# Kernel tuning notes

Hardware: AMD Instinct MI355X
Metric: run time of the kernel (lower is better)

The kernel has to match this reference:

```python
import jax, jax.numpy as jnp
import numpy as np

N, E, D, H_ATT = 10000, 640000, 128, 64


def setup_inputs() -> dict:
    key = jax.random.key(0)
    ks = jax.random.split(key, 8)
    s = 1.0 / np.sqrt(D)
    return {
        "x": jax.random.normal(ks[0], (N, D), jnp.float32),
        "row": jax.random.randint(ks[1], (E,), 0, N, dtype=jnp.int32),
        "col": jax.random.randint(ks[2], (E,), 0, N, dtype=jnp.int32),
        "W1": jax.random.normal(ks[3], (D, D), jnp.float32) * s,
        "b1": jnp.zeros((D,), jnp.float32),
        "W2": jax.random.normal(ks[4], (D, D), jnp.float32) * s,
        "b2": jnp.zeros((D,), jnp.float32),
        "A1": jax.random.normal(ks[5], (D, H_ATT), jnp.float32) * s,
        "ab1": jnp.zeros((H_ATT,), jnp.float32),
        "A2": jax.random.normal(ks[6], (H_ATT, 1), jnp.float32) * (1.0 / np.sqrt(H_ATT)),
    }


def _cos_sim(a, b):
    # torch.cosine_similarity with eps=1e-8
    num = jnp.sum(a * b, axis=-1)
    den = jnp.maximum(jnp.linalg.norm(a, axis=-1) * jnp.linalg.norm(b, axis=-1), 1e-8)
    return num / den


def _euclid(a, b):
    # nn.PairwiseDistance(p=2)
    return jnp.sqrt(jnp.sum((a - b) ** 2, axis=-1) + 1e-12)


def _gcn(x, ew, row, col, W, b):
    # PyG GCNConv: add self loops (weight 1), symmetric normalization, SpMM.
    n = x.shape[0]
    loop = jnp.arange(n, dtype=row.dtype)
    r = jnp.concatenate([row, loop])  # target
    c = jnp.concatenate([col, loop])  # source
    w = jnp.concatenate([ew, jnp.ones((n,), x.dtype)])
    deg = jax.ops.segment_sum(w, r, num_segments=n)
    dis = jnp.where(deg > 0, jax.lax.rsqrt(jnp.maximum(deg, 1e-12)), 0.0)
    norm = dis[r] * w * dis[c]  # [E+N]
    h = x @ W  # [N, out]
    out = jax.ops.segment_sum(norm[:, None] * h[c], r, num_segments=n)
    return out + b


def reference(x, row, col, W1, b1, W2, b2, A1, ab1, A2):
    # --- cosine branch ---
    w = _cos_sim(x[row], x[col])
    x1 = jax.nn.relu(_gcn(x, w, row, col, W1, b1))
    w = _cos_sim(x1[row], x1[col])
    x1 = _gcn(x1, w, row, col, W2, b2)
    # --- euclidean branch ---
    w = _euclid(x[row], x[col])
    x2 = jax.nn.relu(_gcn(x, w, row, col, W1, b1))
    w = _euclid(x2[row], x2[col])
    x2 = _gcn(x2, w, row, col, W2, b2)
    # --- semantic attention fusion ---
    emb = jnp.stack([x1, x2], axis=1)  # [N, 2, D]
    score = jnp.tanh(emb @ A1 + ab1) @ A2  # [N, 2, 1]
    beta = jax.nn.softmax(score, axis=1)
    return jnp.sum(beta * emb, axis=1)  # [N, D]
```

## Files before the change

### kernel.cpp

```cpp
#include <hip/hip_runtime.h>
#include <cstdint>
#include <cstddef>

#define DF 128
#define HATT 64
#define SL 64
#define RPB 1280

static inline int divup(int a, int b) { return (a + b - 1) / b; }

typedef int vint4 __attribute__((ext_vector_type(4)));
typedef unsigned short vus4 __attribute__((ext_vector_type(4)));

static __device__ __forceinline__ unsigned short f2bf(float f) {
    unsigned int u = __float_as_uint(f);
    u = (u + 0x7FFFu + ((u >> 16) & 1u)) >> 16;
    return (unsigned short)u;
}
static __device__ __forceinline__ float bf2f(unsigned short b) {
    return __uint_as_float(((unsigned int)b) << 16);
}

__global__ __launch_bounds__(256) void hist2_kernel(const int* __restrict__ row,
                                                    int* __restrict__ cnt2,
                                                    int E, int n, int ranges, int rpb, int es) {
    int rb = blockIdx.x % ranges;
    int s  = blockIdx.x / ranges;
    int lo = rb * rpb, hi = min(lo + rpb, n);
    int rows = hi - lo;
    __shared__ int lc[RPB];
    for (int j = threadIdx.x; j < rows; j += 256) lc[j] = 0;
    __syncthreads();
    int i0 = s * es, i1 = min(i0 + es, E);
    const vint4* rv = (const vint4*)row;
    for (int j = i0 / 4 + threadIdx.x; j < i1 / 4; j += 256) {
        vint4 r4 = __builtin_nontemporal_load(rv + j);
        if (r4.x >= lo && r4.x < hi) atomicAdd(&lc[r4.x - lo], 1);
        if (r4.y >= lo && r4.y < hi) atomicAdd(&lc[r4.y - lo], 1);
        if (r4.z >= lo && r4.z < hi) atomicAdd(&lc[r4.z - lo], 1);
        if (r4.w >= lo && r4.w < hi) atomicAdd(&lc[r4.w - lo], 1);
    }
    __syncthreads();
    for (int j = threadIdx.x; j < rows; j += 256) cnt2[(size_t)s * n + lo + j] = lc[j];
}

__global__ __launch_bounds__(256) void scanRT_kernel(int* __restrict__ cnt2,
                                                     int* __restrict__ tot, int n) {
    __shared__ int tile[SL][65];
    int r0 = blockIdx.x * 64;
    int w = threadIdx.x >> 6;
    int lane = threadIdx.x & 63;
    int rows = min(64, n - r0);
    for (int s = w; s < SL; s += 4) {
        int v = (lane < rows) ? cnt2[(size_t)s * n + r0 + lane] : 0;
        tile[s][lane] = v;
    }
    __syncthreads();
    int t = threadIdx.x;
    if (t < rows) {
        int run = 0;
#pragma unroll
        for (int s = 0; s < SL; ++s) {
            int v = tile[s][t];
            tile[s][t] = run;
            run += v;
        }
        tot[r0 + t] = run;
    }
    __syncthreads();
    for (int s = w; s < SL; s += 4) {
        if (lane < rows) cnt2[(size_t)s * n + r0 + lane] = tile[s][lane];
    }
}

__global__ __launch_bounds__(1024) void scanT_kernel(const int* __restrict__ tot,
                                                     int* __restrict__ row_ptr, int n) {
    __shared__ int sums[1024];
    int t = threadIdx.x;
    int chunk = (n + 1023) >> 10;
    int start = t * chunk, end = min(start + chunk, n);
    int s = 0;
    for (int r = start; r < end; ++r) s += tot[r];
    sums[t] = s;
    __syncthreads();
    for (int off = 1; off < 1024; off <<= 1) {
        int v = (t >= off) ? sums[t - off] : 0;
        __syncthreads();
        sums[t] += v;
        __syncthreads();
    }
    int run = sums[t] - s;
    for (int r = start; r < end; ++r) {
        row_ptr[r] = run;
        run += tot[r];
    }
    if (t == 1023) row_ptr[n] = sums[1023];
}

__global__ __launch_bounds__(256) void scatter2_kernel(const int* __restrict__ row,
                                                       const int* __restrict__ col,
                                                       const int* __restrict__ cnt2,
                                                       const int* __restrict__ row_ptr,
                                                       unsigned short* __restrict__ col_s,
                                                       int E, int n, int ranges, int rpb, int es) {
    int rb = blockIdx.x % ranges;
    int s  = blockIdx.x / ranges;
    int lo = rb * rpb, hi = min(lo + rpb, n);
    int rows = hi - lo;
    __shared__ int cur[RPB];
    for (int j = threadIdx.x; j < rows; j += 256)
        cur[j] = cnt2[(size_t)s * n + lo + j] + row_ptr[lo + j];
    __syncthreads();
    int i0 = s * es, i1 = min(i0 + es, E);
    const vint4* rv = (const vint4*)row;
    const vint4* cv = (const vint4*)col;
    for (int j = i0 / 4 + threadIdx.x; j < i1 / 4; j += 256) {
        vint4 r4 = __builtin_nontemporal_load(rv + j);
        bool b0 = (r4.x >= lo && r4.x < hi);
        bool b1 = (r4.y >= lo && r4.y < hi);
        bool b2 = (r4.z >= lo && r4.z < hi);
        bool b3 = (r4.w >= lo && r4.w < hi);
        if (b0 | b1 | b2 | b3) {
            vint4 c4 = __builtin_nontemporal_load(cv + j);
            if (b0) { int p = atomicAdd(&cur[r4.x - lo], 1); col_s[p] = (unsigned short)c4.x; }
            if (b1) { int p = atomicAdd(&cur[r4.y - lo], 1); col_s[p] = (unsigned short)c4.y; }
            if (b2) { int p = atomicAdd(&cur[r4.z - lo], 1); col_s[p] = (unsigned short)c4.z; }
            if (b3) { int p = atomicAdd(&cur[r4.w - lo], 1); col_s[p] = (unsigned short)c4.w; }
        }
    }
}

__global__ __launch_bounds__(256) void split_x_kernel(const float* __restrict__ x,
                                                      float* __restrict__ xA,
                                                      float* __restrict__ xB,
                                                      float* __restrict__ sqn, int n) {
    int wid = (blockIdx.x * blockDim.x + threadIdx.x) >> 6;
    int lane = threadIdx.x & 63;
    if (wid >= n) return;
    float v0 = x[(size_t)wid * DF + lane];
    float v1 = x[(size_t)wid * DF + 64 + lane];
    xA[(size_t)wid * 64 + lane] = v0;
    xB[(size_t)wid * 64 + lane] = v1;
    float s = v0 * v0 + v1 * v1;
    for (int off = 32; off; off >>= 1) s += __shfl_xor(s, off);
    if (lane == 0) sqn[wid] = s;
}

__global__ __launch_bounds__(256) void edgewA_kernel(const float* __restrict__ tA,
                                                     const unsigned short* __restrict__ col_s,
                                                     const int* __restrict__ row_ptr,
                                                     float* __restrict__ dpart, int n) {
    int wid = (blockIdx.x * blockDim.x + threadIdx.x) >> 6;
    int lane = threadIdx.x & 63;
    if (wid >= n) return;
    int sub = lane & 15, g = lane >> 4;
    int s = row_ptr[wid], e = row_ptr[wid + 1];
    float4 a = ((const float4*)(tA + (size_t)wid * 64))[sub];
    for (int base = s; base < e; base += 64) {
        int m = e - base; if (m > 64) m = 64;
        int cc = 0;
        if (lane < m) cc = (int)col_s[base + lane];
        float dkeep = 0.f;
#define EWA_BODY(CHK)                                                        \
        _Pragma("unroll")                                                    \
        for (int it = 0; it < 16; ++it) {                                    \
            int idx = g * 16 + it;                                           \
            int c = __shfl(cc, idx);                                         \
            if (CHK) {                                                       \
                float4 b = ((const float4*)(tA + (size_t)c * 64))[sub];      \
                float d = a.x * b.x + a.y * b.y + a.z * b.z + a.w * b.w;     \
                d += __shfl_xor(d, 8); d += __shfl_xor(d, 4);                \
                d += __shfl_xor(d, 2); d += __shfl_xor(d, 1);                \
                dkeep = (sub == it) ? d : dkeep;                             \
            }                                                                \
        }
        if (m == 64) { EWA_BODY(true) } else { EWA_BODY(idx < m) }
#undef EWA_BODY
        if (lane < m) dpart[base + lane] = dkeep;
    }
}

__global__ __launch_bounds__(256) void edgewB1_kernel(const float* __restrict__ tB,
                                                      const float* __restrict__ sqn,
                                                      const unsigned short* __restrict__ col_s,
                                                      const int* __restrict__ row_ptr,
                                                      const float* __restrict__ dpart,
                                                      float* __restrict__ wA,
                                                      float* __restrict__ wB,
                                                      float* __restrict__ disA,
                                                      float* __restrict__ disB, int n) {
    int wid = (blockIdx.x * blockDim.x + threadIdx.x) >> 6;
    int lane = threadIdx.x & 63;
    if (wid >= n) return;
    int sub = lane & 15, g = lane >> 4;
    int s = row_ptr[wid], e = row_ptr[wid + 1];
    float4 a = ((const float4*)(tB + (size_t)wid * 64))[sub];
    float na = sqn[wid];
    float accA = 0.f, accB = 0.f;
    for (int base = s; base < e; base += 64) {
        int m = e - base; if (m > 64) m = 64;
        int cc = 0; float dp = 0.f;
        if (lane < m) {
            cc = (int)col_s[base + lane];
            dp = dpart[base + lane];
        }
        float dkeep = 0.f;
#define EWB1_BODY(CHK)                                                       \
        _Pragma("unroll")                                                    \
        for (int it = 0; it < 16; ++it) {                                    \
            int idx = g * 16 + it;                                           \
            int c = __shfl(cc, idx);                                         \
            if (CHK) {                                                       \
                float4 b = ((const float4*)(tB + (size_t)c * 64))[sub];      \
                float d = a.x * b.x + a.y * b.y + a.z * b.z + a.w * b.w;     \
                d += __shfl_xor(d, 8); d += __shfl_xor(d, 4);                \
                d += __shfl_xor(d, 2); d += __shfl_xor(d, 1);                \
                dkeep = (sub == it) ? d : dkeep;                             \
            }                                                                \
        }
        if (m == 64) { EWB1_BODY(true) } else { EWB1_BODY(idx < m) }
#undef EWB1_BODY
        if (lane < m) {
            float d = dkeep + dp;
            float nb = sqn[cc];
            float cw = d / fmaxf(sqrtf(na * nb), 1e-8f);
            float ew = sqrtf(fmaxf(na + nb - 2.f * d, 0.f) + 1e-12f);
            wA[base + lane] = cw;
            wB[base + lane] = ew;
            accA += cw;
            accB += ew;
        }
    }
#pragma unroll
    for (int off = 32; off; off >>= 1) {
        accA += __shfl_xor(accA, off);
        accB += __shfl_xor(accB, off);
    }
    if (lane == 0) {
        float dA = 1.f + accA;
        disA[wid] = (dA > 0.f) ? rsqrtf(fmaxf(dA, 1e-12f)) : 0.f;
        float dB = 1.f + accB;
        disB[wid] = (dB > 0.f) ? rsqrtf(fmaxf(dB, 1e-12f)) : 0.f;
    }
}

__global__ __launch_bounds__(256) void edgewA2_kernel(const float* __restrict__ t0,
                                                      const float* __restrict__ t1,
                                                      const unsigned short* __restrict__ col_s,
                                                      const int* __restrict__ row_ptr,
                                                      float* __restrict__ dp0,
                                                      float* __restrict__ dp1, int n) {
    int br = blockIdx.x & 1;
    int wid = (blockIdx.x >> 1) * 4 + (threadIdx.x >> 6);
    int lane = threadIdx.x & 63;
    if (wid >= n) return;
    const float* tA = br ? t1 : t0;
    float* dpart = br ? dp1 : dp0;
    int sub = lane & 15, g = lane >> 4;
    int s = row_ptr[wid], e = row_ptr[wid + 1];
    float4 a = ((const float4*)(tA + (size_t)wid * 64))[sub];
    for (int base = s; base < e; base += 64) {
        int m = e - base; if (m > 64) m = 64;
        int cc = 0;
        if (lane < m) cc = (int)col_s[base + lane];
        float dkeep = 0.f;
#define EWA2_BODY(CHK)                                                       \
        _Pragma("unroll")                                                    \
        for (int it = 0; it < 16; ++it) {                                    \
            int idx = g * 16 + it;                                           \
            int c = __shfl(cc, idx);                                         \
            if (CHK) {                                                       \
                float4 b = ((const float4*)(tA + (size_t)c * 64))[sub];      \
                float d = a.x * b.x + a.y * b.y + a.z * b.z + a.w * b.w;     \
                d += __shfl_xor(d, 8); d += __shfl_xor(d, 4);                \
                d += __shfl_xor(d, 2); d += __shfl_xor(d, 1);                \
                dkeep = (sub == it) ? d : dkeep;                             \
            }                                                                \
        }
        if (m == 64) { EWA2_BODY(true) } else { EWA2_BODY(idx < m) }
#undef EWA2_BODY
        if (lane < m) dpart[base + lane] = dkeep;
    }
}

__global__ __launch_bounds__(256) void edgewB2_kernel(const float* __restrict__ t0B,
                                                      const float* __restrict__ t1B,
                                                      const float* __restrict__ sq1pA,
                                                      const float* __restrict__ sq1pB,
                                                      const float* __restrict__ sq2pA,
                                                      const float* __restrict__ sq2pB,
                                                      const unsigned short* __restrict__ col_s,
                                                      const int* __restrict__ row_ptr,
                                                      const float* __restrict__ dp0,
                                                      const float* __restrict__ dp1,
                                                      float* __restrict__ wsA,
                                                      float* __restrict__ wsB,
                                                      float* __restrict__ disA,
                                                      float* __restrict__ disB, int n) {
    int br = blockIdx.x & 1;
    int wid = (blockIdx.x >> 1) * 4 + (threadIdx.x >> 6);
    int lane = threadIdx.x & 63;
    if (wid >= n) return;
    const float* tB = br ? t1B : t0B;
    const float* sqA = br ? sq2pA : sq1pA;
    const float* sqB = br ? sq2pB : sq1pB;
    const float* dpart = br ? dp1 : dp0;
    float* wOut = br ? wsB : wsA;
    float* disOut = br ? disB : disA;
    int sub = lane & 15, g = lane >> 4;
    int s = row_ptr[wid], e = row_ptr[wid + 1];
    float4 a = ((const float4*)(tB + (size_t)wid * 64))[sub];
    float na = sqA[wid] + sqB[wid];
    float acc = 0.f;
    for (int base = s; base < e; base += 64) {
        int m = e - base; if (m > 64) m = 64;
        int cc = 0; float dp = 0.f;
        if (lane < m) {
            cc = (int)col_s[base + lane];
            dp = dpart[base + lane];
        }
        float dkeep = 0.f;
#define EWB2_BODY(CHK)                                                       \
        _Pragma("unroll")                                                    \
        for (int it = 0; it < 16; ++it) {                                    \
            int idx = g * 16 + it;                                           \
            int c = __shfl(cc, idx);                                         \
            if (CHK) {                                                       \
                float4 b = ((const float4*)(tB + (size_t)c * 64))[sub];      \
                float d = a.x * b.x + a.y * b.y + a.z * b.z + a.w * b.w;     \
                d += __shfl_xor(d, 8); d += __shfl_xor(d, 4);                \
                d += __shfl_xor(d, 2); d += __shfl_xor(d, 1);                \
                dkeep = (sub == it) ? d : dkeep;                             \
            }                                                                \
        }
        if (m == 64) { EWB2_BODY(true) } else { EWB2_BODY(idx < m) }
#undef EWB2_BODY
        if (lane < m) {
            float d = dkeep + dp;
            float nb = sqA[cc] + sqB[cc];
            float w;
            if (br == 0) w = d / fmaxf(sqrtf(na * nb), 1e-8f);
            else w = sqrtf(fmaxf(na + nb - 2.f * d, 0.f) + 1e-12f);
            wOut[base + lane] = w;
            acc += w;
        }
    }
#pragma unroll
    for (int off = 32; off; off >>= 1) acc += __shfl_xor(acc, off);
    if (lane == 0) {
        float dg = 1.f + acc;
        disOut[wid] = (dg > 0.f) ? rsqrtf(fmaxf(dg, 1e-12f)) : 0.f;
    }
}

__global__ __launch_bounds__(256) void mm_kernel(const float* __restrict__ inA,
                                                 const float* __restrict__ inB,
                                                 int strideIn,
                                                 const float* __restrict__ W,
                                                 unsigned short* __restrict__ hA,
                                                 unsigned short* __restrict__ hB, int n) {
    int wid = (blockIdx.x * blockDim.x + threadIdx.x) >> 6;
    int lane = threadIdx.x & 63;
    int i0 = wid * 4;
    if (i0 >= n) return;
    float v0[4], v1[4];
#pragma unroll
    for (int r = 0; r < 4; ++r) {
        int i = i0 + r;
        if (i < n) { v0[r] = inA[(size_t)i * strideIn + lane]; v1[r] = inB[(size_t)i * strideIn + lane]; }
        else { v0[r] = 0.f; v1[r] = 0.f; }
    }
    float acc0[4] = {0.f, 0.f, 0.f, 0.f};
    float acc1[4] = {0.f, 0.f, 0.f, 0.f};
#pragma unroll 4
    for (int k = 0; k < 64; ++k) {
        float w0 = W[k * DF + lane];
        float w1 = W[k * DF + 64 + lane];
#pragma unroll
        for (int r = 0; r < 4; ++r) {
            float a = __shfl(v0[r], k);
            acc0[r] = fmaf(a, w0, acc0[r]);
            acc1[r] = fmaf(a, w1, acc1[r]);
        }
    }
#pragma unroll 4
    for (int k = 0; k < 64; ++k) {
        float w0 = W[(k + 64) * DF + lane];
        float w1 = W[(k + 64) * DF + 64 + lane];
#pragma unroll
        for (int r = 0; r < 4; ++r) {
            float a = __shfl(v1[r], k);
            acc0[r] = fmaf(a, w0, acc0[r]);
            acc1[r] = fmaf(a, w1, acc1[r]);
        }
    }
#pragma unroll
    for (int r = 0; r < 4; ++r) {
        int i = i0 + r;
        if (i < n) {
            hA[(size_t)i * 64 + lane] = f2bf(acc0[r]);
            hB[(size_t)i * 64 + lane] = f2bf(acc1[r]);
        }
    }
}

__global__ __launch_bounds__(256) void mm2_kernel(const float* __restrict__ x1A_,
                                                  const float* __restrict__ x1B_,
                                                  const float* __restrict__ x2A_,
                                                  const float* __restrict__ x2B_,
                                                  const float* __restrict__ W,
                                                  unsigned short* __restrict__ h1A, unsigned short* __restrict__ h1B,
                                                  unsigned short* __restrict__ h2A, unsigned short* __restrict__ h2B,
                                                  int n) {
    int br = blockIdx.x & 1;
    const float* inA = br ? x2A_ : x1A_;
    const float* inB = br ? x2B_ : x1B_;
    unsigned short* hA = br ? h2A : h1A;
    unsigned short* hB = br ? h2B : h1B;
    int wid = (blockIdx.x >> 1) * 4 + (threadIdx.x >> 6);
    int lane = threadIdx.x & 63;
    int i0 = wid * 4;
    if (i0 >= n) return;
    float v0[4], v1[4];
#pragma unroll
    for (int r = 0; r < 4; ++r) {
        int i = i0 + r;
        if (i < n) { v0[r] = inA[(size_t)i * 64 + lane]; v1[r] = inB[(size_t)i * 64 + lane]; }
        else { v0[r] = 0.f; v1[r] = 0.f; }
    }
    float acc0[4] = {0.f, 0.f, 0.f, 0.f};
    float acc1[4] = {0.f, 0.f, 0.f, 0.f};
#pragma unroll 4
    for (int k = 0; k < 64; ++k) {
        float w0 = W[k * DF + lane];
        float w1 = W[k * DF + 64 + lane];
#pragma unroll
        for (int r = 0; r < 4; ++r) {
            float a = __shfl(v0[r], k);
            acc0[r] = fmaf(a, w0, acc0[r]);
            acc1[r] = fmaf(a, w1, acc1[r]);
        }
    }
#pragma unroll 4
    for (int k = 0; k < 64; ++k) {
        float w0 = W[(k + 64) * DF + lane];
        float w1 = W[(k + 64) * DF + 64 + lane];
#pragma unroll
        for (int r = 0; r < 4; ++r) {
            float a = __shfl(v1[r], k);
            acc0[r] = fmaf(a, w0, acc0[r]);
            acc1[r] = fmaf(a, w1, acc1[r]);
        }
    }
#pragma unroll
    for (int r = 0; r < 4; ++r) {
        int i = i0 + r;
        if (i < n) {
            hA[(size_t)i * 64 + lane] = f2bf(acc0[r]);
            hB[(size_t)i * 64 + lane] = f2bf(acc1[r]);
        }
    }
}

__global__ __launch_bounds__(256) void spmm_l1_kernel(const unsigned short* __restrict__ hA,
                                                      const unsigned short* __restrict__ hB,
                                                      const float* __restrict__ wsA,
                                                      const float* __restrict__ wsB,
                                                      const unsigned short* __restrict__ col_s,
                                                      const float* __restrict__ disA,
                                                      const float* __restrict__ disB,
                                                      const int* __restrict__ row_ptr,
                                                      const float* __restrict__ bias,
                                                      float* __restrict__ x1A, float* __restrict__ x1B,
                                                      float* __restrict__ x2A, float* __restrict__ x2B,
                                                      float* __restrict__ sq1pA, float* __restrict__ sq1pB,
                                                      float* __restrict__ sq2pA, float* __restrict__ sq2pB,
                                                      int n) {
    int half = blockIdx.x & 1;
    int wid = (blockIdx.x >> 1) * 4 + (threadIdx.x >> 6);
    int lane = threadIdx.x & 63;
    if (wid >= n) return;
    const unsigned short* hH = half ? hB : hA;
    float* x1H = half ? x1B : x1A;
    float* x2H = half ? x2B : x2A;
    float* sq1 = half ? sq1pB : sq1pA;
    float* sq2 = half ? sq2pB : sq2pA;
    const float* biasH = bias + half * 64;
    int sub = lane & 15, g = lane >> 4;
    int s = row_ptr[wid], e = row_ptr[wid + 1];
    float diA = disA[wid], diB = disB[wid];
    float4 aA = make_float4(0.f, 0.f, 0.f, 0.f);
    float4 aB = make_float4(0.f, 0.f, 0.f, 0.f);
    for (int base = s; base < e; base += 64) {
        int m = e - base; if (m > 64) m = 64;
        int cc = 0; float wa = 0.f, wb = 0.f;
        if (lane < m) {
            cc = (int)col_s[base + lane];
            wa = wsA[base + lane] * disA[cc];
            wb = wsB[base + lane] * disB[cc];
        }
#define SPL1_BODY(CHK)                                                       \
        _Pragma("unroll")                                                    \
        for (int it = 0; it < 16; ++it) {                                    \
            int idx = it * 4 + g;                                            \
            int c = __shfl(cc, idx);                                         \
            float ceA = __shfl(wa, idx);                                     \
            float ceB = __shfl(wb, idx);                                     \
            if (CHK) {                                                       \
                vus4 gv = ((const vus4*)(hH + (size_t)c * 64))[sub];         \
                float g0 = bf2f(gv.x), g1 = bf2f(gv.y);                      \
                float g2 = bf2f(gv.z), g3 = bf2f(gv.w);                      \
                aA.x = fmaf(ceA, g0, aA.x); aA.y = fmaf(ceA, g1, aA.y);      \
                aA.z = fmaf(ceA, g2, aA.z); aA.w = fmaf(ceA, g3, aA.w);      \
                aB.x = fmaf(ceB, g0, aB.x); aB.y = fmaf(ceB, g1, aB.y);      \
                aB.z = fmaf(ceB, g2, aB.z); aB.w = fmaf(ceB, g3, aB.w);      \
            }                                                                \
        }
        if (m == 64) { SPL1_BODY(true) } else { SPL1_BODY(idx < m) }
#undef SPL1_BODY
    }
#pragma unroll
    for (int off = 16; off <= 32; off <<= 1) {
        aA.x += __shfl_xor(aA.x, off); aA.y += __shfl_xor(aA.y, off);
        aA.z += __shfl_xor(aA.z, off); aA.w += __shfl_xor(aA.w, off);
        aB.x += __shfl_xor(aB.x, off); aB.y += __shfl_xor(aB.y, off);
        aB.z += __shfl_xor(aB.z, off); aB.w += __shfl_xor(aB.w, off);
    }
    vus4 hvb = ((const vus4*)(hH + (size_t)wid * 64))[sub];
    float4 hv = make_float4(bf2f(hvb.x), bf2f(hvb.y), bf2f(hvb.z), bf2f(hvb.w));
    float4 bb = ((const float4*)biasH)[sub];
    float4 oA, oB;
    oA.x = fmaxf(diA * (aA.x + diA * hv.x) + bb.x, 0.f);
    oA.y = fmaxf(diA * (aA.y + diA * hv.y) + bb.y, 0.f);
    oA.z = fmaxf(diA * (aA.z + diA * hv.z) + bb.z, 0.f);
    oA.w = fmaxf(diA * (aA.w + diA * hv.w) + bb.w, 0.f);
    oB.x = fmaxf(diB * (aB.x + diB * hv.x) + bb.x, 0.f);
    oB.y = fmaxf(diB * (aB.y + diB * hv.y) + bb.y, 0.f);
    oB.z = fmaxf(diB * (aB.z + diB * hv.z) + bb.z, 0.f);
    oB.w = fmaxf(diB * (aB.w + diB * hv.w) + bb.w, 0.f);
    if (g == 0) {
        ((float4*)(x1H + (size_t)wid * 64))[sub] = oA;
        ((float4*)(x2H + (size_t)wid * 64))[sub] = oB;
    }
    float sA = oA.x * oA.x + oA.y * oA.y + oA.z * oA.z + oA.w * oA.w;
    float sB = oB.x * oB.x + oB.y * oB.y + oB.z * oB.z + oB.w * oB.w;
#pragma unroll
    for (int off = 8; off; off >>= 1) {
        sA += __shfl_xor(sA, off);
        sB += __shfl_xor(sB, off);
    }
    if (lane == 0) { sq1[wid] = sA; sq2[wid] = sB; }
}

__global__ __launch_bounds__(256) void spmm2q_kernel(const unsigned short* __restrict__ h1A,
                                                     const unsigned short* __restrict__ h1B,
                                                     const unsigned short* __restrict__ h2A,
                                                     const unsigned short* __restrict__ h2B,
                                                     const float* __restrict__ wsA,
                                                     const float* __restrict__ wsB,
                                                     const unsigned short* __restrict__ col_s,
                                                     const float* __restrict__ disA,
                                                     const float* __restrict__ disB,
                                                     const int* __restrict__ row_ptr,
                                                     const float* __restrict__ bias,
                                                     float* __restrict__ x1A, float* __restrict__ x1B,
                                                     float* __restrict__ x2A, float* __restrict__ x2B,
                                                     int n) {
    int sel = blockIdx.x & 3;
    int br = sel & 1;
    int half = sel >> 1;
    const unsigned short* hH = br ? (half ? h2B : h2A) : (half ? h1B : h1A);
    const float* ws = br ? wsB : wsA;
    const float* dis = br ? disB : disA;
    float* outH = br ? (half ? x2B : x2A) : (half ? x1B : x1A);
    const float* biasH = bias + half * 64;
    int wid = (blockIdx.x >> 2) * 4 + (threadIdx.x >> 6);
    int lane = threadIdx.x & 63;
    if (wid >= n) return;
    int sub = lane & 15, g = lane >> 4;
    int s = row_ptr[wid], e = row_ptr[wid + 1];
    float di = dis[wid];
    float4 a = make_float4(0.f, 0.f, 0.f, 0.f);
    for (int base = s; base < e; base += 64) {
        int m = e - base; if (m > 64) m = 64;
        int cc = 0; float wv = 0.f;
        if (lane < m) {
            cc = (int)col_s[base + lane];
            wv = ws[base + lane] * dis[cc];
        }
#define SP2_BODY(CHK)                                                        \
        _Pragma("unroll")                                                    \
        for (int it = 0; it < 16; ++it) {                                    \
            int idx = it * 4 + g;                                            \
            int c = __shfl(cc, idx);                                         \
            float ce = __shfl(wv, idx);                                      \
            if (CHK) {                                                       \
                vus4 gv = ((const vus4*)(hH + (size_t)c * 64))[sub];         \
                a.x = fmaf(ce, bf2f(gv.x), a.x);                             \
                a.y = fmaf(ce, bf2f(gv.y), a.y);                             \
                a.z = fmaf(ce, bf2f(gv.z), a.z);                             \
                a.w = fmaf(ce, bf2f(gv.w), a.w);                             \
            }                                                                \
        }
        if (m == 64) { SP2_BODY(true) } else { SP2_BODY(idx < m) }
#undef SP2_BODY
    }
#pragma unroll
    for (int off = 16; off <= 32; off <<= 1) {
        a.x += __shfl_xor(a.x, off); a.y += __shfl_xor(a.y, off);
        a.z += __shfl_xor(a.z, off); a.w += __shfl_xor(a.w, off);
    }
    if (g == 0) {
        vus4 hvb = ((const vus4*)(hH + (size_t)wid * 64))[sub];
        float4 bb = ((const float4*)biasH)[sub];
        float4 o;
        o.x = di * (a.x + di * bf2f(hvb.x)) + bb.x;
        o.y = di * (a.y + di * bf2f(hvb.y)) + bb.y;
        o.z = di * (a.z + di * bf2f(hvb.z)) + bb.z;
        o.w = di * (a.w + di * bf2f(hvb.w)) + bb.w;
        ((float4*)(outH + (size_t)wid * 64))[sub] = o;
    }
}

__global__ __launch_bounds__(256) void attn_kernel(const float* __restrict__ x1A,
                                                   const float* __restrict__ x1B,
                                                   const float* __restrict__ x2A,
                                                   const float* __restrict__ x2B,
                                                   const float* __restrict__ A1,
                                                   const float* __restrict__ ab1,
                                                   const float* __restrict__ A2,
                                                   float* __restrict__ out, int n) {
    __shared__ float sA1[DF * HATT];
    __shared__ float sA2[HATT];
    __shared__ float sab[HATT];
    int tid = threadIdx.x;
    for (int i = tid; i < DF * HATT; i += 256) sA1[i] = A1[i];
    if (tid < HATT) { sA2[tid] = A2[tid]; sab[tid] = ab1[tid]; }
    __syncthreads();
    int lane = tid & 63;
    int wib = tid >> 6;
    int wid = blockIdx.x * 4 + wib;
    int nw = gridDim.x * 4;
    for (int i = wid; i < n; i += nw) {
        float u0 = x1A[(size_t)i * 64 + lane], u1 = x1B[(size_t)i * 64 + lane];
        float v0 = x2A[(size_t)i * 64 + lane], v1 = x2B[(size_t)i * 64 + lane];
        float acc1 = 0.f, acc2 = 0.f;
#pragma unroll 4
        for (int d = 0; d < 64; ++d) {
            float w = sA1[d * HATT + lane];
            acc1 = fmaf(__shfl(u0, d), w, acc1);
            acc2 = fmaf(__shfl(v0, d), w, acc2);
        }
#pragma unroll 4
        for (int d = 0; d < 64; ++d) {
            float w = sA1[(d + 64) * HATT + lane];
            acc1 = fmaf(__shfl(u1, d), w, acc1);
            acc2 = fmaf(__shfl(v1, d), w, acc2);
        }
        float t1 = tanhf(acc1 + sab[lane]) * sA2[lane];
        float t2 = tanhf(acc2 + sab[lane]) * sA2[lane];
        for (int off = 32; off; off >>= 1) {
            t1 += __shfl_xor(t1, off);
            t2 += __shfl_xor(t2, off);
        }
        float mx = fmaxf(t1, t2);
        float e1 = expf(t1 - mx), e2 = expf(t2 - mx);
        float inv = 1.f / (e1 + e2);
        float be1 = e1 * inv, be2 = e2 * inv;
        out[(size_t)i * DF + lane] = be1 * u0 + be2 * v0;
        out[(size_t)i * DF + 64 + lane] = be1 * u1 + be2 * v1;
    }
}


extern "C" void kernel_launch(void* const* d_in, const int* in_sizes, int n_in,
                              void* d_out, int out_size, void* d_ws, size_t ws_size,
                              hipStream_t stream) {
    const float* x  = (const float*)d_in[0];
    const int* row  = (const int*)d_in[1];
    const int* col  = (const int*)d_in[2];
    const float* W1 = (const float*)d_in[3];
    const float* b1 = (const float*)d_in[4];
    const float* W2 = (const float*)d_in[5];
    const float* b2 = (const float*)d_in[6];
    const float* A1 = (const float*)d_in[7];
    const float* ab1= (const float*)d_in[8];
    const float* A2 = (const float*)d_in[9];
    const int N = in_sizes[0] / DF;
    const int E = in_sizes[1];
    float* out = (float*)d_out;

    char* p = (char*)d_ws;
    auto alloc_b = [&](size_t bytes) -> char* {
        char* r = p;
        p += (bytes + 255) & ~(size_t)255;
        return r;
    };
    float* xA    = (float*)alloc_b((size_t)N * 64 * 4);
    float* xB    = (float*)alloc_b((size_t)N * 64 * 4);
    unsigned short* hA  = (unsigned short*)alloc_b((size_t)N * 64 * 2);
    unsigned short* hB  = (unsigned short*)alloc_b((size_t)N * 64 * 2);
    unsigned short* h2A = (unsigned short*)alloc_b((size_t)N * 64 * 2);
    unsigned short* h2B = (unsigned short*)alloc_b((size_t)N * 64 * 2);
    float* x1A   = (float*)alloc_b((size_t)N * 64 * 4);
    float* x1B   = (float*)alloc_b((size_t)N * 64 * 4);
    float* x2A   = (float*)alloc_b((size_t)N * 64 * 4);
    float* x2B   = (float*)alloc_b((size_t)N * 64 * 4);
    float* wsA   = (float*)alloc_b((size_t)E * 4);
    float* wsB   = (float*)alloc_b((size_t)E * 4);
    float* dp0   = (float*)alloc_b((size_t)E * 4);
    float* dp1   = (float*)alloc_b((size_t)E * 4);
    float* disA  = (float*)alloc_b((size_t)N * 4);
    float* disB  = (float*)alloc_b((size_t)N * 4);
    float* sqnx  = (float*)alloc_b((size_t)N * 4);
    float* sq1pA = (float*)alloc_b((size_t)N * 4);
    float* sq1pB = (float*)alloc_b((size_t)N * 4);
    float* sq2pA = (float*)alloc_b((size_t)N * 4);
    float* sq2pB = (float*)alloc_b((size_t)N * 4);
    int* cnt2    = (int*)alloc_b((size_t)SL * N * 4);
    int* tot     = (int*)alloc_b((size_t)N * 4);
    int* rowptr  = (int*)alloc_b((size_t)(N + 1) * 4);
    unsigned short* col_s = (unsigned short*)alloc_b((size_t)E * 2);
    (void)ws_size; (void)n_in; (void)out_size;

    const int nodeBlocks  = divup(N * 64, 256);
    const int pairBlocks  = 2 * nodeBlocks;
    const int quadBlocks  = 4 * nodeBlocks;
    const int mmBlocks    = divup(divup(N, 4), 4);
    const int mm2Blocks   = 2 * mmBlocks;
    const int ranges = divup(N, RPB);
    const int rpb    = divup(N, ranges);
    int es = divup(E, SL); es = (es + 3) & ~3;
    const int prepBlocks = ranges * SL;

    hist2_kernel<<<prepBlocks, 256, 0, stream>>>(row, cnt2, E, N, ranges, rpb, es);
    split_x_kernel<<<nodeBlocks, 256, 0, stream>>>(x, xA, xB, sqnx, N);
    scanRT_kernel<<<divup(N, 64), 256, 0, stream>>>(cnt2, tot, N);
    scanT_kernel<<<1, 1024, 0, stream>>>(tot, rowptr, N);
    scatter2_kernel<<<prepBlocks, 256, 0, stream>>>(row, col, cnt2, rowptr, col_s, E, N, ranges, rpb, es);

    mm_kernel<<<mmBlocks, 256, 0, stream>>>(x, x + 64, DF, W1, hA, hB, N);

    edgewA_kernel<<<nodeBlocks, 256, 0, stream>>>(xA, col_s, rowptr, dp0, N);
    edgewB1_kernel<<<nodeBlocks, 256, 0, stream>>>(xB, sqnx, col_s, rowptr, dp0,
                                                   wsA, wsB, disA, disB, N);

    spmm_l1_kernel<<<pairBlocks, 256, 0, stream>>>(hA, hB, wsA, wsB, col_s, disA, disB,
                                                   rowptr, b1, x1A, x1B, x2A, x2B,
                                                   sq1pA, sq1pB, sq2pA, sq2pB, N);

    edgewA2_kernel<<<pairBlocks, 256, 0, stream>>>(x1A, x2A, col_s, rowptr, dp0, dp1, N);
    edgewB2_kernel<<<pairBlocks, 256, 0, stream>>>(x1B, x2B, sq1pA, sq1pB, sq2pA, sq2pB,
                                                   col_s, rowptr, dp0, dp1,
                                                   wsA, wsB, disA, disB, N);

    mm2_kernel<<<mm2Blocks, 256, 0, stream>>>(x1A, x1B, x2A, x2B, W2, hA, hB, h2A, h2B, N);

    spmm2q_kernel<<<quadBlocks, 256, 0, stream>>>(hA, hB, h2A, h2B, wsA, wsB, col_s,
                                                  disA, disB, rowptr, b2,
                                                  x1A, x1B, x2A, x2B, N);

    attn_kernel<<<divup(N, 4), 256, 0, stream>>>(x1A, x1B, x2A, x2B, A1, ab1, A2, out, N);
}
```

Before: 356.8 us.

## Merge feature-half splits in SpMM kernels so each wave handles full rows

The layer-1 SpMM now has one wave per node gather both 64-wide halves of h and produce both branch outputs, instead of launching separate blocks per half. The layer-2 SpMM likewise goes from four blocks per node to two, each covering both halves. Squared norms are now reduced in-kernel into a single array per branch, so edgewB2 reads one value per node instead of summing two partials. This removes redundant loads of row_ptr, col indices and edge weights across the split launches, and the per-node partial-norm reads. In exchange it raises register pressure and per-wave work, and reduces the number of waves available to hide gather latency.

```diff
diff --git a/kernel.cpp b/kernel.cpp
--- a/kernel.cpp
+++ b/kernel.cpp
@@ -285,10 +285,8 @@
 
 __global__ __launch_bounds__(256) void edgewB2_kernel(const float* __restrict__ t0B,
                                                       const float* __restrict__ t1B,
-                                                      const float* __restrict__ sq1pA,
-                                                      const float* __restrict__ sq1pB,
-                                                      const float* __restrict__ sq2pA,
-                                                      const float* __restrict__ sq2pB,
+                                                      const float* __restrict__ sqn1,
+                                                      const float* __restrict__ sqn2,
                                                       const unsigned short* __restrict__ col_s,
                                                       const int* __restrict__ row_ptr,
                                                       const float* __restrict__ dp0,
@@ -302,15 +300,14 @@
     int lane = threadIdx.x & 63;
     if (wid >= n) return;
     const float* tB = br ? t1B : t0B;
-    const float* sqA = br ? sq2pA : sq1pA;
-    const float* sqB = br ? sq2pB : sq1pB;
+    const float* sq = br ? sqn2 : sqn1;
     const float* dpart = br ? dp1 : dp0;
     float* wOut = br ? wsB : wsA;
     float* disOut = br ? disB : disA;
     int sub = lane & 15, g = lane >> 4;
     int s = row_ptr[wid], e = row_ptr[wid + 1];
     float4 a = ((const float4*)(tB + (size_t)wid * 64))[sub];
-    float na = sqA[wid] + sqB[wid];
+    float na = sq[wid];
     float acc = 0.f;
     for (int base = s; base < e; base += 64) {
         int m = e - base; if (m > 64) m = 64;
@@ -337,7 +334,7 @@
 #undef EWB2_BODY
         if (lane < m) {
             float d = dkeep + dp;
-            float nb = sqA[cc] + sqB[cc];
+            float nb = sq[cc];
             float w;
             if (br == 0) w = d / fmaxf(sqrtf(na * nb), 1e-8f);
             else w = sqrtf(fmaxf(na + nb - 2.f * d, 0.f) + 1e-12f);
@@ -473,24 +470,18 @@
                                                       const float* __restrict__ bias,
                                                       float* __restrict__ x1A, float* __restrict__ x1B,
                                                       float* __restrict__ x2A, float* __restrict__ x2B,
-                                                      float* __restrict__ sq1pA, float* __restrict__ sq1pB,
-                                                      float* __restrict__ sq2pA, float* __restrict__ sq2pB,
+                                                      float* __restrict__ sqn1, float* __restrict__ sqn2,
                                                       int n) {
-    int half = blockIdx.x & 1;
-    int wid = (blockIdx.x >> 1) * 4 + (threadIdx.x >> 6);
+    int wid = (blockIdx.x * blockDim.x + threadIdx.x) >> 6;
     int lane = threadIdx.x & 63;
     if (wid >= n) return;
-    const unsigned short* hH = half ? hB : hA;
-    float* x1H = half ? x1B : x1A;
-    float* x2H = half ? x2B : x2A;
-    float* sq1 = half ? sq1pB : sq1pA;
-    float* sq2 = half ? sq2pB : sq2pA;
-    const float* biasH = bias + half * 64;
     int sub = lane & 15, g = lane >> 4;
     int s = row_ptr[wid], e = row_ptr[wid + 1];
     float diA = disA[wid], diB = disB[wid];
-    float4 aA = make_float4(0.f, 0.f, 0.f, 0.f);
-    float4 aB = make_float4(0.f, 0.f, 0.f, 0.f);
+    float4 a1A = make_float4(0.f, 0.f, 0.f, 0.f);
+    float4 a1B = make_float4(0.f, 0.f, 0.f, 0.f);
+    float4 a2A = make_float4(0.f, 0.f, 0.f, 0.f);
+    float4 a2B = make_float4(0.f, 0.f, 0.f, 0.f);
     for (int base = s; base < e; base += 64) {
         int m = e - base; if (m > 64) m = 64;
         int cc = 0; float wa = 0.f, wb = 0.f;
@@ -507,13 +498,20 @@
             float ceA = __shfl(wa, idx);                                     \
             float ceB = __shfl(wb, idx);                                     \
             if (CHK) {                                                       \
-                vus4 gv = ((const vus4*)(hH + (size_t)c * 64))[sub];         \
-                float g0 = bf2f(gv.x), g1 = bf2f(gv.y);                      \
-                float g2 = bf2f(gv.z), g3 = bf2f(gv.w);                      \
-                aA.x = fmaf(ceA, g0, aA.x); aA.y = fmaf(ceA, g1, aA.y);      \
-                aA.z = fmaf(ceA, g2, aA.z); aA.w = fmaf(ceA, g3, aA.w);      \
-                aB.x = fmaf(ceB, g0, aB.x); aB.y = fmaf(ceB, g1, aB.y);      \
-                aB.z = fmaf(ceB, g2, aB.z); aB.w = fmaf(ceB, g3, aB.w);      \
+                vus4 gA = ((const vus4*)(hA + (size_t)c * 64))[sub];         \
+                vus4 gB = ((const vus4*)(hB + (size_t)c * 64))[sub];         \
+                float fa0 = bf2f(gA.x), fa1 = bf2f(gA.y);                    \
+                float fa2 = bf2f(gA.z), fa3 = bf2f(gA.w);                    \
+                float fb0 = bf2f(gB.x), fb1 = bf2f(gB.y);                    \
+                float fb2 = bf2f(gB.z), fb3 = bf2f(gB.w);                    \
+                a1A.x = fmaf(ceA, fa0, a1A.x); a1A.y = fmaf(ceA, fa1, a1A.y);\
+                a1A.z = fmaf(ceA, fa2, a1A.z); a1A.w = fmaf(ceA, fa3, a1A.w);\
+                a1B.x = fmaf(ceA, fb0, a1B.x); a1B.y = fmaf(ceA, fb1, a1B.y);\
+                a1B.z = fmaf(ceA, fb2, a1B.z); a1B.w = fmaf(ceA, fb3, a1B.w);\
+                a2A.x = fmaf(ceB, fa0, a2A.x); a2A.y = fmaf(ceB, fa1, a2A.y);\
+                a2A.z = fmaf(ceB, fa2, a2A.z); a2A.w = fmaf(ceB, fa3, a2A.w);\
+                a2B.x = fmaf(ceB, fb0, a2B.x); a2B.y = fmaf(ceB, fb1, a2B.y);\
+                a2B.z = fmaf(ceB, fb2, a2B.z); a2B.w = fmaf(ceB, fb3, a2B.w);\
             }                                                                \
         }
         if (m == 64) { SPL1_BODY(true) } else { SPL1_BODY(idx < m) }
@@ -521,38 +519,57 @@
     }
 #pragma unroll
     for (int off = 16; off <= 32; off <<= 1) {
-        aA.x += __shfl_xor(aA.x, off); aA.y += __shfl_xor(aA.y, off);
-        aA.z += __shfl_xor(aA.z, off); aA.w += __shfl_xor(aA.w, off);
-        aB.x += __shfl_xor(aB.x, off); aB.y += __shfl_xor(aB.y, off);
-        aB.z += __shfl_xor(aB.z, off); aB.w += __shfl_xor(aB.w, off);
-    }
-    vus4 hvb = ((const vus4*)(hH + (size_t)wid * 64))[sub];
-    float4 hv = make_float4(bf2f(hvb.x), bf2f(hvb.y), bf2f(hvb.z), bf2f(hvb.w));
-    float4 bb = ((const float4*)biasH)[sub];
-    float4 oA, oB;
-    oA.x = fmaxf(diA * (aA.x + diA * hv.x) + bb.x, 0.f);
-    oA.y = fmaxf(diA * (aA.y + diA * hv.y) + bb.y, 0.f);
-    oA.z = fmaxf(diA * (aA.z + diA * hv.z) + bb.z, 0.f);
-    oA.w = fmaxf(diA * (aA.w + diA * hv.w) + bb.w, 0.f);
-    oB.x = fmaxf(diB * (aB.x + diB * hv.x) + bb.x, 0.f);
-    oB.y = fmaxf(diB * (aB.y + diB * hv.y) + bb.y, 0.f);
-    oB.z = fmaxf(diB * (aB.z + diB * hv.z) + bb.z, 0.f);
-    oB.w = fmaxf(diB * (aB.w + diB * hv.w) + bb.w, 0.f);
+        a1A.x += __shfl_xor(a1A.x, off); a1A.y += __shfl_xor(a1A.y, off);
+        a1A.z += __shfl_xor(a1A.z, off); a1A.w += __shfl_xor(a1A.w, off);
+        a1B.x += __shfl_xor(a1B.x, off); a1B.y += __shfl_xor(a1B.y, off);
+        a1B.z += __shfl_xor(a1B.z, off); a1B.w += __shfl_xor(a1B.w, off);
+        a2A.x += __shfl_xor(a2A.x, off); a2A.y += __shfl_xor(a2A.y, off);
+        a2A.z += __shfl_xor(a2A.z, off); a2A.w += __shfl_xor(a2A.w, off);
+        a2B.x += __shfl_xor(a2B.x, off); a2B.y += __shfl_xor(a2B.y, off);
+        a2B.z += __shfl_xor(a2B.z, off); a2B.w += __shfl_xor(a2B.w, off);
+    }
+    vus4 hvAb = ((const vus4*)(hA + (size_t)wid * 64))[sub];
+    vus4 hvBb = ((const vus4*)(hB + (size_t)wid * 64))[sub];
+    float4 hvA = make_float4(bf2f(hvAb.x), bf2f(hvAb.y), bf2f(hvAb.z), bf2f(hvAb.w));
+    float4 hvB = make_float4(bf2f(hvBb.x), bf2f(hvBb.y), bf2f(hvBb.z), bf2f(hvBb.w));
+    float4 bbA = ((const float4*)bias)[sub];
+    float4 bbB = ((const float4*)(bias + 64))[sub];
+    float4 o1A, o1B, o2A, o2B;
+    o1A.x = fmaxf(diA * (a1A.x + diA * hvA.x) + bbA.x, 0.f);
+    o1A.y = fmaxf(diA * (a1A.y + diA * hvA.y) + bbA.y, 0.f);
+    o1A.z = fmaxf(diA * (a1A.z + diA * hvA.z) + bbA.z, 0.f);
+    o1A.w = fmaxf(diA * (a1A.w + diA * hvA.w) + bbA.w, 0.f);
+    o1B.x = fmaxf(diA * (a1B.x + diA * hvB.x) + bbB.x, 0.f);
+    o1B.y = fmaxf(diA * (a1B.y + diA * hvB.y) + bbB.y, 0.f);
+    o1B.z = fmaxf(diA * (a1B.z + diA * hvB.z) + bbB.z, 0.f);
+    o1B.w = fmaxf(diA * (a1B.w + diA * hvB.w) + bbB.w, 0.f);
+    o2A.x = fmaxf(diB * (a2A.x + diB * hvA.x) + bbA.x, 0.f);
+    o2A.y = fmaxf(diB * (a2A.y + diB * hvA.y) + bbA.y, 0.f);
+    o2A.z = fmaxf(diB * (a2A.z + diB * hvA.z) + bbA.z, 0.f);
+    o2A.w = fmaxf(diB * (a2A.w + diB * hvA.w) + bbA.w, 0.f);
+    o2B.x = fmaxf(diB * (a2B.x + diB * hvB.x) + bbB.x, 0.f);
+    o2B.y = fmaxf(diB * (a2B.y + diB * hvB.y) + bbB.y, 0.f);
+    o2B.z = fmaxf(diB * (a2B.z + diB * hvB.z) + bbB.z, 0.f);
+    o2B.w = fmaxf(diB * (a2B.w + diB * hvB.w) + bbB.w, 0.f);
     if (g == 0) {
-        ((float4*)(x1H + (size_t)wid * 64))[sub] = oA;
-        ((float4*)(x2H + (size_t)wid * 64))[sub] = oB;
-    }
-    float sA = oA.x * oA.x + oA.y * oA.y + oA.z * oA.z + oA.w * oA.w;
-    float sB = oB.x * oB.x + oB.y * oB.y + oB.z * oB.z + oB.w * oB.w;
+        ((float4*)(x1A + (size_t)wid * 64))[sub] = o1A;
+        ((float4*)(x1B + (size_t)wid * 64))[sub] = o1B;
+        ((float4*)(x2A + (size_t)wid * 64))[sub] = o2A;
+        ((float4*)(x2B + (size_t)wid * 64))[sub] = o2B;
+    }
+    float s1 = o1A.x * o1A.x + o1A.y * o1A.y + o1A.z * o1A.z + o1A.w * o1A.w
+             + o1B.x * o1B.x + o1B.y * o1B.y + o1B.z * o1B.z + o1B.w * o1B.w;
+    float s2 = o2A.x * o2A.x + o2A.y * o2A.y + o2A.z * o2A.z + o2A.w * o2A.w
+             + o2B.x * o2B.x + o2B.y * o2B.y + o2B.z * o2B.z + o2B.w * o2B.w;
 #pragma unroll
     for (int off = 8; off; off >>= 1) {
-        sA += __shfl_xor(sA, off);
-        sB += __shfl_xor(sB, off);
-    }
-    if (lane == 0) { sq1[wid] = sA; sq2[wid] = sB; }
-}
-
-__global__ __launch_bounds__(256) void spmm2q_kernel(const unsigned short* __restrict__ h1A,
+        s1 += __shfl_xor(s1, off);
+        s2 += __shfl_xor(s2, off);
+    }
+    if (lane == 0) { sqn1[wid] = s1; sqn2[wid] = s2; }
+}
+
+__global__ __launch_bounds__(256) void spmm2d_kernel(const unsigned short* __restrict__ h1A,
                                                      const unsigned short* __restrict__ h1B,
                                                      const unsigned short* __restrict__ h2A,
                                                      const unsigned short* __restrict__ h2B,
@@ -566,21 +583,21 @@
                                                      float* __restrict__ x1A, float* __restrict__ x1B,
                                                      float* __restrict__ x2A, float* __restrict__ x2B,
                                                      int n) {
-    int sel = blockIdx.x & 3;
-    int br = sel & 1;
-    int half = sel >> 1;
-    const unsigned short* hH = br ? (half ? h2B : h2A) : (half ? h1B : h1A);
+    int br = blockIdx.x & 1;
+    const unsigned short* hHA = br ? h2A : h1A;
+    const unsigned short* hHB = br ? h2B : h1B;
     const float* ws = br ? wsB : wsA;
     const float* dis = br ? disB : disA;
-    float* outH = br ? (half ? x2B : x2A) : (half ? x1B : x1A);
-    const float* biasH = bias + half * 64;
-    int wid = (blockIdx.x >> 2) * 4 + (threadIdx.x >> 6);
+    float* outA = br ? x2A : x1A;
+    float* outB = br ? x2B : x1B;
+    int wid = (blockIdx.x >> 1) * 4 + (threadIdx.x >> 6);
     int lane = threadIdx.x & 63;
     if (wid >= n) return;
     int sub = lane & 15, g = lane >> 4;
     int s = row_ptr[wid], e = row_ptr[wid + 1];
     float di = dis[wid];
-    float4 a = make_float4(0.f, 0.f, 0.f, 0.f);
+    float4 aA = make_float4(0.f, 0.f, 0.f, 0.f);
+    float4 aB = make_float4(0.f, 0.f, 0.f, 0.f);
     for (int base = s; base < e; base += 64) {
         int m = e - base; if (m > 64) m = 64;
         int cc = 0; float wv = 0.f;
@@ -595,11 +612,16 @@
             int c = __shfl(cc, idx);                                         \
             float ce = __shfl(wv, idx);                                      \
             if (CHK) {                                                       \
-                vus4 gv = ((const vus4*)(hH + (size_t)c * 64))[sub];         \
-                a.x = fmaf(ce, bf2f(gv.x), a.x);                             \
-                a.y = fmaf(ce, bf2f(gv.y), a.y);                             \
-                a.z = fmaf(ce, bf2f(gv.z), a.z);                             \
-                a.w = fmaf(ce, bf2f(gv.w), a.w);                             \
+                vus4 gA = ((const vus4*)(hHA + (size_t)c * 64))[sub];        \
+                vus4 gB = ((const vus4*)(hHB + (size_t)c * 64))[sub];        \
+                aA.x = fmaf(ce, bf2f(gA.x), aA.x);                           \
+                aA.y = fmaf(ce, bf2f(gA.y), aA.y);                           \
+                aA.z = fmaf(ce, bf2f(gA.z), aA.z);                           \
+                aA.w = fmaf(ce, bf2f(gA.w), aA.w);                           \
+                aB.x = fmaf(ce, bf2f(gB.x), aB.x);                           \
+                aB.y = fmaf(ce, bf2f(gB.y), aB.y);                           \
+                aB.z = fmaf(ce, bf2f(gB.z), aB.z);                           \
+                aB.w = fmaf(ce, bf2f(gB.w), aB.w);                           \
             }                                                                \
         }
         if (m == 64) { SP2_BODY(true) } else { SP2_BODY(idx < m) }
@@ -607,18 +629,27 @@
     }
 #pragma unroll
     for (int off = 16; off <= 32; off <<= 1) {
-        a.x += __shfl_xor(a.x, off); a.y += __shfl_xor(a.y, off);
-        a.z += __shfl_xor(a.z, off); a.w += __shfl_xor(a.w, off);
+        aA.x += __shfl_xor(aA.x, off); aA.y += __shfl_xor(aA.y, off);
+        aA.z += __shfl_xor(aA.z, off); aA.w += __shfl_xor(aA.w, off);
+        aB.x += __shfl_xor(aB.x, off); aB.y += __shfl_xor(aB.y, off);
+        aB.z += __shfl_xor(aB.z, off); aB.w += __shfl_xor(aB.w, off);
     }
     if (g == 0) {
-        vus4 hvb = ((const vus4*)(hH + (size_t)wid * 64))[sub];
-        float4 bb = ((const float4*)biasH)[sub];
-        float4 o;
-        o.x = di * (a.x + di * bf2f(hvb.x)) + bb.x;
-        o.y = di * (a.y + di * bf2f(hvb.y)) + bb.y;
-        o.z = di * (a.z + di * bf2f(hvb.z)) + bb.z;
-        o.w = di * (a.w + di * bf2f(hvb.w)) + bb.w;
-        ((float4*)(outH + (size_t)wid * 64))[sub] = o;
+        vus4 hvAb = ((const vus4*)(hHA + (size_t)wid * 64))[sub];
+        vus4 hvBb = ((const vus4*)(hHB + (size_t)wid * 64))[sub];
+        float4 bbA = ((const float4*)bias)[sub];
+        float4 bbB = ((const float4*)(bias + 64))[sub];
+        float4 oA, oB;
+        oA.x = di * (aA.x + di * bf2f(hvAb.x)) + bbA.x;
+        oA.y = di * (aA.y + di * bf2f(hvAb.y)) + bbA.y;
+        oA.z = di * (aA.z + di * bf2f(hvAb.z)) + bbA.z;
+        oA.w = di * (aA.w + di * bf2f(hvAb.w)) + bbA.w;
+        oB.x = di * (aB.x + di * bf2f(hvBb.x)) + bbB.x;
+        oB.y = di * (aB.y + di * bf2f(hvBb.y)) + bbB.y;
+        oB.z = di * (aB.z + di * bf2f(hvBb.z)) + bbB.z;
+        oB.w = di * (aB.w + di * bf2f(hvBb.w)) + bbB.w;
+        ((float4*)(outA + (size_t)wid * 64))[sub] = oA;
+        ((float4*)(outB + (size_t)wid * 64))[sub] = oB;
     }
 }
 
@@ -713,10 +744,8 @@
     float* disA  = (float*)alloc_b((size_t)N * 4);
     float* disB  = (float*)alloc_b((size_t)N * 4);
     float* sqnx  = (float*)alloc_b((size_t)N * 4);
-    float* sq1pA = (float*)alloc_b((size_t)N * 4);
-    float* sq1pB = (float*)alloc_b((size_t)N * 4);
-    float* sq2pA = (float*)alloc_b((size_t)N * 4);
-    float* sq2pB = (float*)alloc_b((size_t)N * 4);
+    float* sqn1  = (float*)alloc_b((size_t)N * 4);
+    float* sqn2  = (float*)alloc_b((size_t)N * 4);
     int* cnt2    = (int*)alloc_b((size_t)SL * N * 4);
     int* tot     = (int*)alloc_b((size_t)N * 4);
     int* rowptr  = (int*)alloc_b((size_t)(N + 1) * 4);
@@ -725,7 +754,6 @@
 
     const int nodeBlocks  = divup(N * 64, 256);
     const int pairBlocks  = 2 * nodeBlocks;
-    const int quadBlocks  = 4 * nodeBlocks;
     const int mmBlocks    = divup(divup(N, 4), 4);
     const int mm2Blocks   = 2 * mmBlocks;
     const int ranges = divup(N, RPB);
@@ -745,18 +773,18 @@
     edgewB1_kernel<<<nodeBlocks, 256, 0, stream>>>(xB, sqnx, col_s, rowptr, dp0,
                                                    wsA, wsB, disA, disB, N);
 
-    spmm_l1_kernel<<<pairBlocks, 256, 0, stream>>>(hA, hB, wsA, wsB, col_s, disA, disB,
+    spmm_l1_kernel<<<nodeBlocks, 256, 0, stream>>>(hA, hB, wsA, wsB, col_s, disA, disB,
                                                    rowptr, b1, x1A, x1B, x2A, x2B,
-                                                   sq1pA, sq1pB, sq2pA, sq2pB, N);
+                                                   sqn1, sqn2, N);
 
     edgewA2_kernel<<<pairBlocks, 256, 0, stream>>>(x1A, x2A, col_s, rowptr, dp0, dp1, N);
-    edgewB2_kernel<<<pairBlocks, 256, 0, stream>>>(x1B, x2B, sq1pA, sq1pB, sq2pA, sq2pB,
+    edgewB2_kernel<<<pairBlocks, 256, 0, stream>>>(x1B, x2B, sqn1, sqn2,
                                                    col_s, rowptr, dp0, dp1,
                                                    wsA, wsB, disA, disB, N);
 
     mm2_kernel<<<mm2Blocks, 256, 0, stream>>>(x1A, x1B, x2A, x2B, W2, hA, hB, h2A, h2B, N);
 
-    spmm2q_kernel<<<quadBlocks, 256, 0, stream>>>(hA, hB, h2A, h2B, wsA, wsB, col_s,
+    spmm2d_kernel<<<pairBlocks, 256, 0, stream>>>(hA, hB, h2A, h2B, wsA, wsB, col_s,
                                                   disA, disB, rowptr, b2,
                                                   x1A, x1B, x2A, x2B, N);
 
```

After: 349.4 us. -2.1%, faster.
